# Kernel optimization log

Measured on AMD Instinct MI355X. Metric: run time of the kernel, lower is better.

Reference implementation:

```python
import jax, jax.numpy as jnp
import numpy as np

V = 256      # vocab_size (hard-coded in source)
H = 2048     # hidden_size
S = 2048     # encoder input length
T = 2048     # decoder target length


def _gru_cell(x, h, w_ih, w_hh, b_ih, b_hh):
    # PyTorch GRU cell math. x, h: [H]; w_ih, w_hh: [3H, H]; b_*: [3H]
    gi = w_ih @ x + b_ih
    gh = w_hh @ h + b_hh
    i_r, i_z, i_n = jnp.split(gi, 3)
    h_r, h_z, h_n = jnp.split(gh, 3)
    r = jax.nn.sigmoid(i_r + h_r)
    z = jax.nn.sigmoid(i_z + h_z)
    n = jnp.tanh(i_n + r * h_n)
    return (1.0 - z) * n + z * h


def setup_inputs() -> dict:
    key = jax.random.key(0)
    ks = jax.random.split(key, 16)
    k = 1.0 / np.sqrt(H)
    u = lambda kk, shape: jax.random.uniform(kk, shape, jnp.float32, -k, k)
    return {
        "inputs": jax.random.randint(ks[0], (S,), 0, V),
        "targets": jax.random.randint(ks[1], (T,), 0, V),
        "emb": jax.random.normal(ks[2], (V, H), jnp.float32),
        "enc_w_ih": u(ks[3], (3 * H, H)),
        "enc_w_hh": u(ks[4], (3 * H, H)),
        "enc_b_ih": u(ks[5], (3 * H,)),
        "enc_b_hh": u(ks[6], (3 * H,)),
        "dec_w_ih": u(ks[7], (3 * H, H)),
        "dec_w_hh": u(ks[8], (3 * H, H)),
        "dec_b_ih": u(ks[9], (3 * H,)),
        "dec_b_hh": u(ks[10], (3 * H,)),
        "fc_w": u(ks[11], (V, H)),
        "fc_b": u(ks[12], (V,)),
    }


def reference(inputs, targets, emb, enc_w_ih, enc_w_hh, enc_b_ih, enc_b_hh,
              dec_w_ih, dec_w_hh, dec_b_ih, dec_b_hh, fc_w, fc_b):
    # Encoder: run GRU over embedded input sequence, keep final state.
    enc_x = emb[inputs]                      # [S, H]
    h0 = jnp.zeros((H,), dtype=emb.dtype)

    def enc_step(h, x):
        return _gru_cell(x, h, enc_w_ih, enc_w_hh, enc_b_ih, enc_b_hh), None

    h_enc, _ = jax.lax.scan(enc_step, h0, enc_x)

    # Decoder token stream: step 0 uses token 0; every later step uses the
    # SAME token targets[1] (faithful to the bug in the original source).
    dec_tokens = jnp.where(jnp.arange(T) == 0, 0, targets[1])  # [T]
    dec_x = emb[dec_tokens]                  # [T, H]

    def dec_step(h, x):
        h_new = _gru_cell(x, h, dec_w_ih, dec_w_hh, dec_b_ih, dec_b_hh)
        return h_new, h_new

    _, dec_hs = jax.lax.scan(dec_step, h_enc, dec_x)  # [T, H]

    # Output projection (batch dim of 1 squeezed away as in the original).
    return dec_hs @ fc_w.T + fc_b            # [T, V]
```

## Files before the change

kernel.cpp:

```cpp
#include <hip/hip_runtime.h>
#include <hip/hip_fp16.h>

#define Hh 2048
#define VV 256
#define SS 2048
#define TT 2048
#define NB 256
#define NT 512

typedef _Float16 h4 __attribute__((ext_vector_type(4)));

__global__ __launch_bounds__(256) void gemm_nt(const float* __restrict__ A,
                                               const float* __restrict__ B,
                                               const float* __restrict__ biasM,
                                               const float* __restrict__ biasN,
                                               float* __restrict__ C,
                                               int M, int N, int K) {
  __shared__ __align__(16) float At[32][68];
  __shared__ __align__(16) float Bt[32][68];
  const int t = threadIdx.x;
  const int m0 = blockIdx.x << 6, n0 = blockIdx.y << 6;
  const int r0 = t >> 3, c4 = (t & 7) << 2;
  const int tm = (t >> 4) << 2, tn = (t & 15) << 2;
  float acc[4][4];
#pragma unroll
  for (int i = 0; i < 4; ++i)
#pragma unroll
    for (int j = 0; j < 4; ++j) acc[i][j] = 0.f;

  for (int k0 = 0; k0 < K; k0 += 32) {
    float4 a0 = *(const float4*)&A[(size_t)(m0 + r0) * K + k0 + c4];
    float4 a1 = *(const float4*)&A[(size_t)(m0 + r0 + 32) * K + k0 + c4];
    float4 b0 = *(const float4*)&B[(size_t)(n0 + r0) * K + k0 + c4];
    float4 b1 = *(const float4*)&B[(size_t)(n0 + r0 + 32) * K + k0 + c4];
    __syncthreads();
    At[c4 + 0][r0] = a0.x; At[c4 + 1][r0] = a0.y; At[c4 + 2][r0] = a0.z; At[c4 + 3][r0] = a0.w;
    At[c4 + 0][r0 + 32] = a1.x; At[c4 + 1][r0 + 32] = a1.y; At[c4 + 2][r0 + 32] = a1.z; At[c4 + 3][r0 + 32] = a1.w;
    Bt[c4 + 0][r0] = b0.x; Bt[c4 + 1][r0] = b0.y; Bt[c4 + 2][r0] = b0.z; Bt[c4 + 3][r0] = b0.w;
    Bt[c4 + 0][r0 + 32] = b1.x; Bt[c4 + 1][r0 + 32] = b1.y; Bt[c4 + 2][r0 + 32] = b1.z; Bt[c4 + 3][r0 + 32] = b1.w;
    __syncthreads();
#pragma unroll
    for (int k = 0; k < 32; ++k) {
      float4 av = *(const float4*)&At[k][tm];
      float4 bv = *(const float4*)&Bt[k][tn];
      acc[0][0] = fmaf(av.x, bv.x, acc[0][0]);
      acc[0][1] = fmaf(av.x, bv.y, acc[0][1]);
      acc[0][2] = fmaf(av.x, bv.z, acc[0][2]);
      acc[0][3] = fmaf(av.x, bv.w, acc[0][3]);
      acc[1][0] = fmaf(av.y, bv.x, acc[1][0]);
      acc[1][1] = fmaf(av.y, bv.y, acc[1][1]);
      acc[1][2] = fmaf(av.y, bv.z, acc[1][2]);
      acc[1][3] = fmaf(av.y, bv.w, acc[1][3]);
      acc[2][0] = fmaf(av.z, bv.x, acc[2][0]);
      acc[2][1] = fmaf(av.z, bv.y, acc[2][1]);
      acc[2][2] = fmaf(av.z, bv.z, acc[2][2]);
      acc[2][3] = fmaf(av.z, bv.w, acc[2][3]);
      acc[3][0] = fmaf(av.w, bv.x, acc[3][0]);
      acc[3][1] = fmaf(av.w, bv.y, acc[3][1]);
      acc[3][2] = fmaf(av.w, bv.z, acc[3][2]);
      acc[3][3] = fmaf(av.w, bv.w, acc[3][3]);
    }
  }
#pragma unroll
  for (int i = 0; i < 4; ++i) {
    float bm = biasM ? biasM[m0 + tm + i] : 0.f;
#pragma unroll
    for (int j = 0; j < 4; ++j) {
      float bn = biasN ? biasN[n0 + tn + j] : 0.f;
      C[(size_t)(m0 + tm + i) * N + n0 + tn + j] = acc[i][j] + bm + bn;
    }
  }
}

__global__ __launch_bounds__(NT) void recur_kernel(
    const float* __restrict__ giT_enc, const float* __restrict__ giT_dec,
    const float* __restrict__ enc_w_hh, const float* __restrict__ enc_b_hh,
    const float* __restrict__ dec_w_hh, const float* __restrict__ dec_b_hh,
    const int* __restrict__ inputs, const int* __restrict__ targets,
    unsigned long long* __restrict__ hb, float* __restrict__ dec_hs) {
  __shared__ __align__(16) _Float16 w_lds[24 * Hh];
  __shared__ __align__(16) float gi_lds[24 * VV];
  __shared__ __align__(16) _Float16 h16[Hh];
  __shared__ __align__(16) unsigned short tok_lds[SS];
  __shared__ float bhh_lds[24];
  __shared__ float gidec_lds[48];

  const int t = threadIdx.x;
  const int b = blockIdx.x;
  const int bks = b << 3;
  const int w = t >> 6, l = t & 63;

  for (int r = 0; r < 24; ++r) {
    const int g = r >> 3, j = r & 7;
    const float* src = enc_w_hh + ((size_t)(g * Hh + bks + j)) * Hh + (t << 2);
    float4 v = *(const float4*)src;
    h4 hv = {(_Float16)v.x, (_Float16)v.y, (_Float16)v.z, (_Float16)v.w};
    *(h4*)&w_lds[(size_t)(j * 3 + g) * Hh + (t << 2)] = hv;
  }
  if (t < 24) bhh_lds[t] = enc_b_hh[(t >> 3) * Hh + bks + (t & 7)];

  for (int r = 0; r < 24; ++r) {
    const int g = r >> 3, j = r & 7;
    const float4* src = (const float4*)(giT_enc + ((size_t)(g * Hh + bks + j)) * VV);
    if (t < 64) ((float4*)&gi_lds[r * VV])[t] = src[t];
  }

  for (int u = t; u < SS; u += NT) tok_lds[u] = (unsigned short)inputs[u];

  if (t < 48) {
    const int sel = t / 24, r = t % 24;
    const int tk = sel ? targets[1] : 0;
    const int g = r >> 3, jj = r & 7;
    gidec_lds[sel * 24 + r] = giT_dec[((size_t)(g * Hh + bks + jj)) * VV + tk];
  }

  if (t < 8) {
    __hip_atomic_store(&hb[bks + t], 1ULL << 32, __ATOMIC_RELAXED,
                       __HIP_MEMORY_SCOPE_AGENT);
  }
  float hprev = 0.0f;

  for (int step = 0; step < SS + TT; ++step) {
    if (step == SS) {
      for (int r = 0; r < 24; ++r) {
        const int g = r >> 3, j = r & 7;
        const float* src = dec_w_hh + ((size_t)(g * Hh + bks + j)) * Hh + (t << 2);
        float4 v = *(const float4*)src;
        h4 hv = {(_Float16)v.x, (_Float16)v.y, (_Float16)v.z, (_Float16)v.w};
        *(h4*)&w_lds[(size_t)(j * 3 + g) * Hh + (t << 2)] = hv;
      }
      if (t < 24) bhh_lds[t] = dec_b_hh[(t >> 3) * Hh + bks + (t & 7)];
    }

    {
      const unsigned long long* src = hb + ((size_t)(step & 1) << 11);
      const unsigned int want = (unsigned int)(step + 1);
      const int s0 = t << 2;
      unsigned long long v0, v1, v2, v3;
      for (;;) {
        v0 = __hip_atomic_load(src + s0 + 0, __ATOMIC_RELAXED, __HIP_MEMORY_SCOPE_AGENT);
        v1 = __hip_atomic_load(src + s0 + 1, __ATOMIC_RELAXED, __HIP_MEMORY_SCOPE_AGENT);
        v2 = __hip_atomic_load(src + s0 + 2, __ATOMIC_RELAXED, __HIP_MEMORY_SCOPE_AGENT);
        v3 = __hip_atomic_load(src + s0 + 3, __ATOMIC_RELAXED, __HIP_MEMORY_SCOPE_AGENT);
        if ((unsigned int)(v0 >> 32) == want && (unsigned int)(v1 >> 32) == want &&
            (unsigned int)(v2 >> 32) == want && (unsigned int)(v3 >> 32) == want)
          break;
        __builtin_amdgcn_s_sleep(1);
      }
      h4 hv = {(_Float16)__uint_as_float((unsigned int)v0),
               (_Float16)__uint_as_float((unsigned int)v1),
               (_Float16)__uint_as_float((unsigned int)v2),
               (_Float16)__uint_as_float((unsigned int)v3)};
      *(h4*)&h16[s0] = hv;
    }
    __syncthreads();

    float ar = 0.f, az = 0.f, an = 0.f;
    const _Float16* wr = &w_lds[(size_t)(w * 3 + 0) * Hh];
    const _Float16* wz = &w_lds[(size_t)(w * 3 + 1) * Hh];
    const _Float16* wn = &w_lds[(size_t)(w * 3 + 2) * Hh];
#pragma unroll
    for (int q = 0; q < 8; ++q) {
      const int c = q * 256 + (l << 2);
      h4 hv = *(const h4*)&h16[c];
      h4 vr = *(const h4*)&wr[c];
      h4 vz = *(const h4*)&wz[c];
      h4 vn = *(const h4*)&wn[c];
      float f0 = (float)hv.x, f1 = (float)hv.y, f2 = (float)hv.z, f3 = (float)hv.w;
      ar = fmaf((float)vr.x, f0, ar); ar = fmaf((float)vr.y, f1, ar);
      ar = fmaf((float)vr.z, f2, ar); ar = fmaf((float)vr.w, f3, ar);
      az = fmaf((float)vz.x, f0, az); az = fmaf((float)vz.y, f1, az);
      az = fmaf((float)vz.z, f2, az); az = fmaf((float)vz.w, f3, az);
      an = fmaf((float)vn.x, f0, an); an = fmaf((float)vn.y, f1, an);
      an = fmaf((float)vn.z, f2, an); an = fmaf((float)vn.w, f3, an);
    }
#pragma unroll
    for (int off = 32; off > 0; off >>= 1) {
      ar += __shfl_xor(ar, off);
      az += __shfl_xor(az, off);
      an += __shfl_xor(an, off);
    }

    if (l == 0) {
      float gr, gz, gn;
      if (step < SS) {
        const int tk = tok_lds[step];
        gr = gi_lds[(0 + w) * VV + tk];
        gz = gi_lds[(8 + w) * VV + tk];
        gn = gi_lds[(16 + w) * VV + tk];
      } else {
        const int sel = (step == SS) ? 0 : 24;
        gr = gidec_lds[sel + w];
        gz = gidec_lds[sel + 8 + w];
        gn = gidec_lds[sel + 16 + w];
      }
      const float xr = gr + ar + bhh_lds[w];
      const float xz = gz + az + bhh_lds[8 + w];
      const float hn = an + bhh_lds[16 + w];
      const float rr = 1.f / (1.f + __expf(-xr));
      const float zz = 1.f / (1.f + __expf(-xz));
      const float nn = tanhf(gn + rr * hn);
      const float hnew = (1.f - zz) * nn + zz * hprev;

      const unsigned long long pk =
          ((unsigned long long)(unsigned int)(step + 2) << 32) |
          (unsigned long long)__float_as_uint(hnew);
      __hip_atomic_store(&hb[(((size_t)((step + 1) & 1)) << 11) + bks + w], pk,
                         __ATOMIC_RELAXED, __HIP_MEMORY_SCOPE_AGENT);
      if (step >= SS) dec_hs[(size_t)(step - SS) * Hh + bks + w] = hnew;
      hprev = hnew;
    }
    __syncthreads();
  }
}

extern "C" void kernel_launch(void* const* d_in, const int* in_sizes, int n_in,
                              void* d_out, int out_size, void* d_ws, size_t ws_size,
                              hipStream_t stream) {
  (void)in_sizes; (void)n_in; (void)out_size; (void)ws_size;
  const int* inputs = (const int*)d_in[0];
  const int* targets = (const int*)d_in[1];
  const float* emb = (const float*)d_in[2];
  const float* enc_w_ih = (const float*)d_in[3];
  const float* enc_w_hh = (const float*)d_in[4];
  const float* enc_b_ih = (const float*)d_in[5];
  const float* enc_b_hh = (const float*)d_in[6];
  const float* dec_w_ih = (const float*)d_in[7];
  const float* dec_w_hh = (const float*)d_in[8];
  const float* dec_b_ih = (const float*)d_in[9];
  const float* dec_b_hh = (const float*)d_in[10];
  const float* fc_w = (const float*)d_in[11];
  const float* fc_b = (const float*)d_in[12];
  float* out = (float*)d_out;

  float* giT_enc = (float*)d_ws;
  float* giT_dec = giT_enc + (size_t)6144 * 256;
  float* dec_hs = giT_dec + (size_t)6144 * 256;
  unsigned long long* hb =
      (unsigned long long*)(dec_hs + (size_t)TT * Hh);

  gemm_nt<<<dim3(96, 4), 256, 0, stream>>>(enc_w_ih, emb, enc_b_ih, nullptr,
                                           giT_enc, 3 * Hh, VV, Hh);
  gemm_nt<<<dim3(96, 4), 256, 0, stream>>>(dec_w_ih, emb, dec_b_ih, nullptr,
                                           giT_dec, 3 * Hh, VV, Hh);

  void* args[] = {&giT_enc, &giT_dec, &enc_w_hh, &enc_b_hh, &dec_w_hh,
                  &dec_b_hh, &inputs, &targets, &hb, &dec_hs};
  hipError_t e = hipLaunchCooperativeKernel((void*)recur_kernel, dim3(NB),
                                            dim3(NT), args, 0, stream);
  if (e != hipSuccess) {
    recur_kernel<<<dim3(NB), dim3(NT), 0, stream>>>(
        giT_enc, giT_dec, enc_w_hh, enc_b_hh, dec_w_hh, dec_b_hh, inputs,
        targets, hb, dec_hs);
  }

  gemm_nt<<<dim3(32, 4), 256, 0, stream>>>(dec_hs, fc_w, nullptr, fc_b, out,
                                           TT, VV, Hh);
}
```

Before: 18.55 ms.

## Keep recurrent weights in registers, pack fp16 state flags, drop per-step barrier

Moves each wave's slice of the hidden-to-hidden weights from LDS into registers as fp16 vectors and uses packed fp16 dot-product instructions for the matvec. The inter-block hidden-state exchange now packs a 16-bit step tag with an fp16 value into 32-bit words and polls them with one cache-bypassing dwordx4 load. The shared h buffer is double-buffered so the trailing __syncthreads can be removed. Together these aim to cut LDS traffic, exchange bandwidth and barrier latency on the serial critical path. In exchange the 16-bit tag and fp16 state add wraparound and precision risk, and the inline asm ties the kernel to this ISA.

Result: slower. 19.13 ms (+3.1%).

```diff
diff --git a/kernel.cpp b/kernel.cpp
--- a/kernel.cpp
+++ b/kernel.cpp
@@ -9,6 +9,19 @@
 #define NT 512
 
 typedef _Float16 h4 __attribute__((ext_vector_type(4)));
+typedef _Float16 h2 __attribute__((ext_vector_type(2)));
+typedef unsigned int u32x4 __attribute__((ext_vector_type(4)));
+typedef unsigned short u16x4 __attribute__((ext_vector_type(4)));
+
+#if defined(__has_builtin)
+#if __has_builtin(__builtin_amdgcn_fdot2)
+#define FDOT2(a, b, c) __builtin_amdgcn_fdot2((a), (b), (c), false)
+#endif
+#endif
+#ifndef FDOT2
+#define FDOT2(a, b, c) \
+  fmaf((float)(a).x, (float)(b).x, fmaf((float)(a).y, (float)(b).y, (c)))
+#endif
 
 __global__ __launch_bounds__(256) void gemm_nt(const float* __restrict__ A,
                                                const float* __restrict__ B,
@@ -77,12 +90,10 @@
     const float* __restrict__ enc_w_hh, const float* __restrict__ enc_b_hh,
     const float* __restrict__ dec_w_hh, const float* __restrict__ dec_b_hh,
     const int* __restrict__ inputs, const int* __restrict__ targets,
-    unsigned long long* __restrict__ hb, float* __restrict__ dec_hs) {
-  __shared__ __align__(16) _Float16 w_lds[24 * Hh];
+    unsigned int* __restrict__ hb, float* __restrict__ dec_hs) {
   __shared__ __align__(16) float gi_lds[24 * VV];
-  __shared__ __align__(16) _Float16 h16[Hh];
+  __shared__ __align__(16) _Float16 h16[2][Hh];
   __shared__ __align__(16) unsigned short tok_lds[SS];
-  __shared__ float bhh_lds[24];
   __shared__ float gidec_lds[48];
 
   const int t = threadIdx.x;
@@ -90,14 +101,24 @@
   const int bks = b << 3;
   const int w = t >> 6, l = t & 63;
 
-  for (int r = 0; r < 24; ++r) {
-    const int g = r >> 3, j = r & 7;
-    const float* src = enc_w_hh + ((size_t)(g * Hh + bks + j)) * Hh + (t << 2);
-    float4 v = *(const float4*)src;
-    h4 hv = {(_Float16)v.x, (_Float16)v.y, (_Float16)v.z, (_Float16)v.w};
-    *(h4*)&w_lds[(size_t)(j * 3 + g) * Hh + (t << 2)] = hv;
-  }
-  if (t < 24) bhh_lds[t] = enc_b_hh[(t >> 3) * Hh + bks + (t & 7)];
+  h4 wreg[24];
+  float br_, bz_, bn_;
+  auto load_wb = [&](const float* W, const float* B) {
+#pragma unroll
+    for (int g = 0; g < 3; ++g) {
+      const float* rb = W + ((size_t)(g * Hh + bks + w)) * Hh + (l << 2);
+#pragma unroll
+      for (int q = 0; q < 8; ++q) {
+        float4 vv = *(const float4*)&rb[q * 256];
+        wreg[g * 8 + q] = h4{(_Float16)vv.x, (_Float16)vv.y,
+                            (_Float16)vv.z, (_Float16)vv.w};
+      }
+    }
+    br_ = B[bks + w];
+    bz_ = B[Hh + bks + w];
+    bn_ = B[2 * Hh + bks + w];
+  };
+  load_wb(enc_w_hh, enc_b_hh);
 
   for (int r = 0; r < 24; ++r) {
     const int g = r >> 3, j = r & 7;
@@ -115,64 +136,53 @@
   }
 
   if (t < 8) {
-    __hip_atomic_store(&hb[bks + t], 1ULL << 32, __ATOMIC_RELAXED,
+    __hip_atomic_store(&hb[bks + t], 0x00010000u, __ATOMIC_RELAXED,
                        __HIP_MEMORY_SCOPE_AGENT);
   }
   float hprev = 0.0f;
 
   for (int step = 0; step < SS + TT; ++step) {
-    if (step == SS) {
-      for (int r = 0; r < 24; ++r) {
-        const int g = r >> 3, j = r & 7;
-        const float* src = dec_w_hh + ((size_t)(g * Hh + bks + j)) * Hh + (t << 2);
-        float4 v = *(const float4*)src;
-        h4 hv = {(_Float16)v.x, (_Float16)v.y, (_Float16)v.z, (_Float16)v.w};
-        *(h4*)&w_lds[(size_t)(j * 3 + g) * Hh + (t << 2)] = hv;
-      }
-      if (t < 24) bhh_lds[t] = dec_b_hh[(t >> 3) * Hh + bks + (t & 7)];
-    }
+    if (step == SS) load_wb(dec_w_hh, dec_b_hh);
+    const int sb = step & 1;
 
     {
-      const unsigned long long* src = hb + ((size_t)(step & 1) << 11);
-      const unsigned int want = (unsigned int)(step + 1);
-      const int s0 = t << 2;
-      unsigned long long v0, v1, v2, v3;
+      const unsigned int* addr = hb + ((size_t)sb << 11) + (t << 2);
+      const unsigned int want = ((unsigned int)(step + 1)) << 16;
+      u32x4 v;
       for (;;) {
-        v0 = __hip_atomic_load(src + s0 + 0, __ATOMIC_RELAXED, __HIP_MEMORY_SCOPE_AGENT);
-        v1 = __hip_atomic_load(src + s0 + 1, __ATOMIC_RELAXED, __HIP_MEMORY_SCOPE_AGENT);
-        v2 = __hip_atomic_load(src + s0 + 2, __ATOMIC_RELAXED, __HIP_MEMORY_SCOPE_AGENT);
-        v3 = __hip_atomic_load(src + s0 + 3, __ATOMIC_RELAXED, __HIP_MEMORY_SCOPE_AGENT);
-        if ((unsigned int)(v0 >> 32) == want && (unsigned int)(v1 >> 32) == want &&
-            (unsigned int)(v2 >> 32) == want && (unsigned int)(v3 >> 32) == want)
+        asm volatile(
+            "global_load_dwordx4 %0, %1, off sc0 sc1\n\t"
+            "s_waitcnt vmcnt(0)"
+            : "=&v"(v)
+            : "v"(addr)
+            : "memory");
+        if ((v.x & 0xFFFF0000u) == want && (v.y & 0xFFFF0000u) == want &&
+            (v.z & 0xFFFF0000u) == want && (v.w & 0xFFFF0000u) == want)
           break;
         __builtin_amdgcn_s_sleep(1);
       }
-      h4 hv = {(_Float16)__uint_as_float((unsigned int)v0),
-               (_Float16)__uint_as_float((unsigned int)v1),
-               (_Float16)__uint_as_float((unsigned int)v2),
-               (_Float16)__uint_as_float((unsigned int)v3)};
-      *(h4*)&h16[s0] = hv;
+      u16x4 hu = {(unsigned short)v.x, (unsigned short)v.y,
+                  (unsigned short)v.z, (unsigned short)v.w};
+      *(u16x4*)&h16[sb][t << 2] = hu;
     }
     __syncthreads();
 
     float ar = 0.f, az = 0.f, an = 0.f;
-    const _Float16* wr = &w_lds[(size_t)(w * 3 + 0) * Hh];
-    const _Float16* wz = &w_lds[(size_t)(w * 3 + 1) * Hh];
-    const _Float16* wn = &w_lds[(size_t)(w * 3 + 2) * Hh];
 #pragma unroll
     for (int q = 0; q < 8; ++q) {
       const int c = q * 256 + (l << 2);
-      h4 hv = *(const h4*)&h16[c];
-      h4 vr = *(const h4*)&wr[c];
-      h4 vz = *(const h4*)&wz[c];
-      h4 vn = *(const h4*)&wn[c];
-      float f0 = (float)hv.x, f1 = (float)hv.y, f2 = (float)hv.z, f3 = (float)hv.w;
-      ar = fmaf((float)vr.x, f0, ar); ar = fmaf((float)vr.y, f1, ar);
-      ar = fmaf((float)vr.z, f2, ar); ar = fmaf((float)vr.w, f3, ar);
-      az = fmaf((float)vz.x, f0, az); az = fmaf((float)vz.y, f1, az);
-      az = fmaf((float)vz.z, f2, az); az = fmaf((float)vz.w, f3, az);
-      an = fmaf((float)vn.x, f0, an); an = fmaf((float)vn.y, f1, an);
-      an = fmaf((float)vn.z, f2, an); an = fmaf((float)vn.w, f3, an);
+      h4 hv = *(const h4*)&h16[sb][c];
+      h2 hlo = __builtin_shufflevector(hv, hv, 0, 1);
+      h2 hhi = __builtin_shufflevector(hv, hv, 2, 3);
+      h4 wr4 = wreg[q];
+      h4 wz4 = wreg[8 + q];
+      h4 wn4 = wreg[16 + q];
+      ar = FDOT2(__builtin_shufflevector(wr4, wr4, 0, 1), hlo, ar);
+      ar = FDOT2(__builtin_shufflevector(wr4, wr4, 2, 3), hhi, ar);
+      az = FDOT2(__builtin_shufflevector(wz4, wz4, 0, 1), hlo, az);
+      az = FDOT2(__builtin_shufflevector(wz4, wz4, 2, 3), hhi, az);
+      an = FDOT2(__builtin_shufflevector(wn4, wn4, 0, 1), hlo, an);
+      an = FDOT2(__builtin_shufflevector(wn4, wn4, 2, 3), hhi, an);
     }
 #pragma unroll
     for (int off = 32; off > 0; off >>= 1) {
@@ -194,23 +204,23 @@
         gz = gidec_lds[sel + 8 + w];
         gn = gidec_lds[sel + 16 + w];
       }
-      const float xr = gr + ar + bhh_lds[w];
-      const float xz = gz + az + bhh_lds[8 + w];
-      const float hn = an + bhh_lds[16 + w];
+      const float xr = gr + ar + br_;
+      const float xz = gz + az + bz_;
+      const float hn = an + bn_;
       const float rr = 1.f / (1.f + __expf(-xr));
       const float zz = 1.f / (1.f + __expf(-xz));
       const float nn = tanhf(gn + rr * hn);
       const float hnew = (1.f - zz) * nn + zz * hprev;
 
-      const unsigned long long pk =
-          ((unsigned long long)(unsigned int)(step + 2) << 32) |
-          (unsigned long long)__float_as_uint(hnew);
+      _Float16 hf = (_Float16)hnew;
+      const unsigned int pk =
+          (((unsigned int)(step + 2)) << 16) |
+          (unsigned int)__builtin_bit_cast(unsigned short, hf);
       __hip_atomic_store(&hb[(((size_t)((step + 1) & 1)) << 11) + bks + w], pk,
                          __ATOMIC_RELAXED, __HIP_MEMORY_SCOPE_AGENT);
       if (step >= SS) dec_hs[(size_t)(step - SS) * Hh + bks + w] = hnew;
       hprev = hnew;
     }
-    __syncthreads();
   }
 }
 
@@ -236,8 +246,8 @@
   float* giT_enc = (float*)d_ws;
   float* giT_dec = giT_enc + (size_t)6144 * 256;
   float* dec_hs = giT_dec + (size_t)6144 * 256;
-  unsigned long long* hb =
-      (unsigned long long*)(dec_hs + (size_t)TT * Hh);
+  unsigned int* hb =
+      (unsigned int*)(dec_hs + (size_t)TT * Hh);
 
   gemm_nt<<<dim3(96, 4), 256, 0, stream>>>(enc_w_ih, emb, enc_b_ih, nullptr,
                                            giT_enc, 3 * Hh, VV, Hh);
```
